# Optimization experiments

Hardware: AMD Instinct MI355X
Metric: run time of the kernel (lower is better)

The kernel has to match this reference:

```python
import jax, jax.numpy as jnp
import numpy as np

B, L, D, H, FF = 2, 2048, 1024, 16, 4096


def _xavier(key, out_d, in_d):
    lim = (6.0 / (in_d + out_d)) ** 0.5
    return jax.random.uniform(key, (out_d, in_d), jnp.float32, -lim, lim)


def setup_inputs() -> dict:
    key = jax.random.key(0)
    ks = jax.random.split(key, 7)
    x = jax.random.normal(ks[0], (B, L, D), dtype=jnp.float32)
    wq = _xavier(ks[1], D, D)
    wk = _xavier(ks[2], D, D)
    wv = _xavier(ks[3], D, D)
    wo = _xavier(ks[4], D, D)
    w1 = _xavier(ks[5], FF, D)
    w2 = _xavier(ks[6], D, FF)
    zD = jnp.zeros((D,), jnp.float32)
    return dict(x=x, wq=wq, bq=zD, wk=wk, bk=zD, wv=wv, bv=zD, wo=wo, bo=zD,
                w1=w1, b1=jnp.zeros((FF,), jnp.float32), w2=w2, b2=zD)


def _ln2d(x, eps=1e-5):
    # F.layer_norm(x, x.shape[1:]): normalize jointly over (L, D), no affine
    mu = jnp.mean(x, axis=(1, 2), keepdims=True)
    var = jnp.var(x, axis=(1, 2), keepdims=True)
    return (x - mu) * jax.lax.rsqrt(var + eps)


def reference(x, wq, bq, wk, bk, wv, bv, wo, bo, w1, b1, w2, b2):
    Bx, Lx, Dx = x.shape
    nH = H
    Dh = Dx // nH
    h = _ln2d(x)
    q = (h @ wq.T + bq).reshape(Bx, Lx, nH, Dh).transpose(0, 2, 1, 3)  # (B,H,L,Dh)
    k = (h @ wk.T + bk).reshape(Bx, Lx, nH, Dh).transpose(0, 2, 1, 3)
    v = (h @ wv.T + bv).reshape(Bx, Lx, nH, Dh).transpose(0, 2, 1, 3)
    # NOTE: faithful to source bug: scale = 1/sqrt(key.size(dim=1)) = 1/sqrt(num_heads)
    scale = 1.0 / jnp.sqrt(jnp.asarray(nH, jnp.float32))
    att = jax.nn.softmax(jnp.einsum('bhqd,bhkd->bhqk', q, k) * scale, axis=-1)
    o = jnp.einsum('bhqk,bhkd->bhqd', att, v).transpose(0, 2, 1, 3).reshape(Bx, Lx, Dx)
    o = o @ wo.T + bo
    y = _ln2d(o + x)
    ff = jax.nn.relu(y @ w1.T + b1) @ w2.T + b2
    return ff + x  # second residual adds the ORIGINAL x (as in source)
```

## Files before the change

kernel.cpp:

```cpp
#include <hip/hip_runtime.h>
#include <cstdint>
#include <cstddef>

typedef unsigned short u16;
typedef unsigned int uint;
typedef __bf16 bf16x8 __attribute__((ext_vector_type(8)));
typedef float f32x4 __attribute__((ext_vector_type(4)));

#define BATCH 2
#define SEQ 2048
#define DIM 1024
#define NH 16
#define DH 64
#define FFD 4096
#define MROWS 4096
#define PER_BATCH 2097152

__device__ __forceinline__ u16 f2b(float f) {
  uint u = __builtin_bit_cast(uint, f);
  u += 0x7FFFu + ((u >> 16) & 1u);
  return (u16)(u >> 16);
}

__device__ __forceinline__ uint pkbf2(float a, float b) {
  u16 x = __builtin_bit_cast(u16, (__bf16)a);
  u16 y = __builtin_bit_cast(u16, (__bf16)b);
  return (uint)x | ((uint)y << 16);
}

__device__ __forceinline__ int xcd_swz(int flat, int nwg) {
  return (flat & 7) * (nwg >> 3) + (flat >> 3);
}

#define GLL(gp, lp)                                                            \
  __builtin_amdgcn_global_load_lds(                                            \
      (const __attribute__((address_space(1))) void*)(gp),                     \
      (__attribute__((address_space(3))) void*)(lp), 16, 0, 0)

__global__ __launch_bounds__(256) void cvt4_kernel(const float* __restrict__ s0,
                                                   const float* __restrict__ s1,
                                                   const float* __restrict__ s2,
                                                   const float* __restrict__ s3,
                                                   u16* d0, u16* d1, u16* d2, u16* d3,
                                                   int n) {
  int t = blockIdx.y;
  const float* src = (t == 0) ? s0 : (t == 1) ? s1 : (t == 2) ? s2 : s3;
  u16* dst = (t == 0) ? d0 : (t == 1) ? d1 : (t == 2) ? d2 : d3;
  int i = (blockIdx.x * 256 + threadIdx.x) * 8;
  if (i >= n) return;
  float4 a = *(const float4*)(src + i);
  float4 b = *(const float4*)(src + i + 4);
  uint4 o;
  o.x = f2b(a.x) | ((uint)f2b(a.y) << 16);
  o.y = f2b(a.z) | ((uint)f2b(a.w) << 16);
  o.z = f2b(b.x) | ((uint)f2b(b.y) << 16);
  o.w = f2b(b.z) | ((uint)f2b(b.w) << 16);
  *(uint4*)(dst + i) = o;
}

__global__ __launch_bounds__(256) void reduce_stats_kernel(const float* __restrict__ x,
                                                           float* __restrict__ stats) {
  int b = blockIdx.y;
  const float* p = x + (size_t)b * PER_BATCH;
  float s = 0.f, ss = 0.f;
  int stride = gridDim.x * 256 * 4;
  for (int i = (blockIdx.x * 256 + threadIdx.x) * 4; i < PER_BATCH; i += stride) {
    float4 v = *(const float4*)(p + i);
    s  += (v.x + v.y) + (v.z + v.w);
    ss += (v.x * v.x + v.y * v.y) + (v.z * v.z + v.w * v.w);
  }
#pragma unroll
  for (int m = 32; m; m >>= 1) { s += __shfl_xor(s, m); ss += __shfl_xor(ss, m); }
  __shared__ float red[16];
  int w = threadIdx.x >> 6;
  if ((threadIdx.x & 63) == 0) { red[w] = s; red[8 + w] = ss; }
  __syncthreads();
  if (threadIdx.x == 0) {
    atomicAdd(&stats[b * 2],     red[0] + red[1] + red[2] + red[3]);
    atomicAdd(&stats[b * 2 + 1], red[8] + red[9] + red[10] + red[11]);
  }
}

__global__ __launch_bounds__(256) void ln_apply_kernel(const float* __restrict__ xin,
                                                       const float* __restrict__ stats,
                                                       u16* __restrict__ out) {
  int i = (blockIdx.x * 256 + threadIdx.x) * 4;
  int b = i >> 21;
  const float inv = 1.f / (float)PER_BATCH;
  float mu = stats[b * 2] * inv;
  float var = stats[b * 2 + 1] * inv - mu * mu;
  float rs = rsqrtf(var + 1e-5f);
  float4 v = *(const float4*)(xin + i);
  uint r0 = f2b((v.x - mu) * rs) | ((uint)f2b((v.y - mu) * rs) << 16);
  uint r1 = f2b((v.z - mu) * rs) | ((uint)f2b((v.w - mu) * rs) << 16);
  *(uint2*)(out + i) = make_uint2(r0, r1);
}

template <int TN, int RELU, int RESID, int OUTBF, int TRV, int DBUF>
__device__ __forceinline__ void gemm_bt_body(const u16* __restrict__ A,
                                             const u16* __restrict__ Bm,
                                             const float* __restrict__ bias,
                                             const float* __restrict__ resid,
                                             void* __restrict__ Cout,
                                             int M, int N, int K,
                                             int m0, int n0, float oscale) {
  constexpr int AI  = (TN == 128) ? 4 : 2;
  constexpr int BCH = (TN == 128) ? 4 : 2;
  constexpr int NB  = DBUF ? 2 : 1;
  __shared__ __align__(16) u16 As[NB][128 * 64];
  __shared__ __align__(16) u16 Bs[NB][TN * 64];
  const int tid = threadIdx.x;
  const int lane = tid & 63, w = tid >> 6;
  const int wr = (TN == 128) ? (w >> 1) : w;
  const int wc = (TN == 128) ? (w & 1) : 0;
  const int ln = lane & 15, qd = lane >> 4;

  f32x4 acc[AI][4] = {};

  const int lrow = lane >> 3;
  const int scl  = (lane & 7) ^ lrow;
  const u16* Ag = A  + (size_t)(m0 + w * 32 + lrow) * K + scl * 8;
  const u16* Bg = Bm + (size_t)(n0 + w * 8 * BCH + lrow) * K + scl * 8;

  const int co0 = ((qd)     ^ (ln & 7)) * 8;
  const int co1 = ((4 + qd) ^ (ln & 7)) * 8;

  auto STAGE = [&](int buf, int k0) {
#pragma unroll
    for (int r = 0; r < 4; ++r)
      GLL(Ag + (size_t)(r * 8) * K + k0, As[buf] + (w * 4 + r) * 512);
#pragma unroll
    for (int r = 0; r < BCH; ++r)
      GLL(Bg + (size_t)(r * 8) * K + k0, Bs[buf] + (w * BCH + r) * 512);
  };

  auto COMPUTE = [&](int buf) {
#pragma unroll
    for (int kk = 0; kk < 2; ++kk) {
      const int co = kk ? co1 : co0;
      bf16x8 af[AI], bf[4];
#pragma unroll
      for (int t = 0; t < AI; ++t)
        af[t] = *(const bf16x8*)&As[buf][(wr * (AI * 16) + t * 16 + ln) * 64 + co];
#pragma unroll
      for (int t = 0; t < 4; ++t)
        bf[t] = *(const bf16x8*)&Bs[buf][(wc * 64 + t * 16 + ln) * 64 + co];
#pragma unroll
      for (int i = 0; i < AI; ++i)
#pragma unroll
        for (int j = 0; j < 4; ++j)
          acc[i][j] = __builtin_amdgcn_mfma_f32_16x16x32_bf16(af[i], bf[j], acc[i][j], 0, 0, 0);
    }
  };

  if constexpr (NB == 2) {
    const int nk = K >> 6;
    STAGE(0, 0);
    for (int t = 0; t < nk; ++t) {
      const int p = t & 1;
      __syncthreads();
      if (t + 1 < nk) STAGE(1 - p, (t + 1) * 64);
      COMPUTE(p);
    }
  } else {
    for (int k0 = 0; k0 < K; k0 += 64) {
      __syncthreads();
      STAGE(0, k0);
      __syncthreads();
      COMPUTE(0);
    }
  }

#pragma unroll
  for (int i = 0; i < AI; ++i) {
    int row = m0 + wr * (AI * 16) + i * 16 + qd * 4;
#pragma unroll
    for (int j = 0; j < 4; ++j) {
      int col = n0 + wc * 64 + j * 16 + ln;
      float bv = bias[col];
      if (TRV) {
        union { uint2 u2; u16 us[4]; } pk;
#pragma unroll
        for (int r = 0; r < 4; ++r) pk.us[r] = f2b(acc[i][j][r] + bv);
        *(uint2*)&((u16*)Cout)[(size_t)col * MROWS + row] = pk.u2;
      } else {
#pragma unroll
        for (int r = 0; r < 4; ++r) {
          float v = (acc[i][j][r] + bv) * oscale;
          if (RELU) v = fmaxf(v, 0.f);
          size_t off = (size_t)(row + r) * N + col;
          if (RESID) v += resid[off];
          if (OUTBF) ((u16*)Cout)[off] = f2b(v);
          else       ((float*)Cout)[off] = v;
        }
      }
    }
  }
}

template <int TN, int RELU, int RESID, int OUTBF, int DBUF>
__global__ __launch_bounds__(256) void gemm_bt_kernel(const u16* __restrict__ A,
                                                      const u16* __restrict__ Bm,
                                                      const float* __restrict__ bias,
                                                      const float* __restrict__ resid,
                                                      void* __restrict__ Cout,
                                                      int M, int N, int K) {
  const int nx = gridDim.x;
  const int nwg = nx * gridDim.y;
  const int wid = xcd_swz(blockIdx.x + nx * blockIdx.y, nwg);
  gemm_bt_body<TN, RELU, RESID, OUTBF, 0, DBUF>(A, Bm, bias, resid, Cout, M, N, K,
                                                (wid / nx) * 128, (wid % nx) * TN, 1.0f);
}

__global__ __launch_bounds__(256) void gemm_qkv_kernel(const u16* __restrict__ A,
                                                       const u16* B0, const u16* B1, const u16* B2,
                                                       const float* c0, const float* c1, const float* c2,
                                                       u16* o0, u16* o1, u16* o2) {
  int z = blockIdx.z;
  const int wid = xcd_swz(blockIdx.x + 8 * blockIdx.y, 256);
  const int m0 = (wid >> 3) * 128, n0 = (wid & 7) * 128;
  if (z == 2) {
    gemm_bt_body<128, 0, 0, 1, 1, 0>(A, B2, c2, nullptr, o2, MROWS, DIM, DIM,
                                     m0, n0, 1.0f);
  } else {
    const u16* Bm = (z == 0) ? B0 : B1;
    const float* bias = (z == 0) ? c0 : c1;
    u16* Cout = (z == 0) ? o0 : o1;
    float sc = (z == 0) ? 0.25f : 1.0f;
    gemm_bt_body<128, 0, 0, 1, 0, 0>(A, Bm, bias, nullptr, Cout, MROWS, DIM, DIM,
                                     m0, n0, sc);
  }
}

__global__ __launch_bounds__(256, 2) void attn_kernel(const u16* __restrict__ Q,
                                                      const u16* __restrict__ Km,
                                                      const u16* __restrict__ vT,
                                                      u16* __restrict__ O) {
  __shared__ __align__(16) u16 Ks[2][64 * 64];
  __shared__ __align__(16) u16 Vt[2][64 * 64];
  __shared__ __align__(16) u16 Ps[4][32 * 64];

  const int tid = threadIdx.x, lane = tid & 63, w = tid >> 6;
  const int ln = lane & 15, qd = lane >> 4;
  const int flat = blockIdx.x + 16 * (blockIdx.y + 16 * blockIdx.z);
  const int wid = xcd_swz(flat, 512);
  const int qi = wid & 15, head = (wid >> 4) & 15, b = wid >> 8;
  const int wq0 = b * SEQ + qi * 128 + w * 32;
  const int hcol = head * DH;

  bf16x8 qf[2][2];
#pragma unroll
  for (int ti = 0; ti < 2; ++ti)
#pragma unroll
    for (int kk = 0; kk < 2; ++kk)
      qf[ti][kk] = *(const bf16x8*)&Q[(size_t)(wq0 + ti * 16 + ln) * DIM + hcol + kk * 32 + qd * 8];

  union { u16 u[8]; bf16x8 v; } oneu;
#pragma unroll
  for (int e = 0; e < 8; ++e) oneu.u[e] = 0x3F80;
  const bf16x8 vones = oneu.v;

  f32x4 accO[2][4] = {};
  f32x4 accL[2] = {};

  const int srow = lane >> 3;
  const int scl  = (lane & 7) ^ srow;
  const u16* Kg = Km + (size_t)(b * SEQ + w * 16 + srow) * DIM + hcol + scl * 8;
  const u16* Vg = vT + (size_t)(hcol + w * 16 + srow) * MROWS + b * SEQ + scl * 8;
  u16* Pw = Ps[w];
  const int swz = ln & 7;

#pragma unroll
  for (int r = 0; r < 2; ++r) {
    GLL(Kg + (size_t)(r * 8) * DIM,   &Ks[0][(w * 2 + r) * 512]);
    GLL(Vg + (size_t)(r * 8) * MROWS, &Vt[0][(w * 2 + r) * 512]);
  }

  for (int t = 0; t < SEQ / 64; ++t) {
    const int p = t & 1;
    const int kt = t * 64;
    __syncthreads();

    if (t + 1 < SEQ / 64) {
      const int kt2 = kt + 64;
#pragma unroll
      for (int r = 0; r < 2; ++r) {
        GLL(Kg + (size_t)(kt2 + r * 8) * DIM,   &Ks[1 - p][(w * 2 + r) * 512]);
        GLL(Vg + (size_t)(r * 8) * MROWS + kt2, &Vt[1 - p][(w * 2 + r) * 512]);
      }
    }

    f32x4 sacc[4][2] = {};
#pragma unroll
    for (int kk = 0; kk < 2; ++kk) {
      bf16x8 kf[4];
#pragma unroll
      for (int tj = 0; tj < 4; ++tj)
        kf[tj] = *(const bf16x8*)&Ks[p][(tj * 16 + ln) * 64 + (((kk * 4 + qd) ^ swz) * 8)];
      __builtin_amdgcn_s_setprio(1);
#pragma unroll
      for (int tj = 0; tj < 4; ++tj)
#pragma unroll
        for (int ti = 0; ti < 2; ++ti)
          sacc[tj][ti] = __builtin_amdgcn_mfma_f32_16x16x32_bf16(kf[tj], qf[ti][kk], sacc[tj][ti], 0, 0, 0);
      __builtin_amdgcn_s_setprio(0);
    }

#pragma unroll
    for (int tj = 0; tj < 4; ++tj)
#pragma unroll
      for (int ti = 0; ti < 2; ++ti) {
        uint lo = pkbf2(__expf(sacc[tj][ti][0]), __expf(sacc[tj][ti][1]));
        uint hi = pkbf2(__expf(sacc[tj][ti][2]), __expf(sacc[tj][ti][3]));
        *(uint2*)&Pw[(ti * 16 + ln) * 64 + (((2 * tj + (qd >> 1)) ^ swz) * 8) + (qd & 1) * 4] =
            make_uint2(lo, hi);
      }

#pragma unroll
    for (int kk = 0; kk < 2; ++kk) {
      bf16x8 pf[2], vf[4];
#pragma unroll
      for (int ti = 0; ti < 2; ++ti)
        pf[ti] = *(const bf16x8*)&Pw[(ti * 16 + ln) * 64 + (((kk * 4 + qd) ^ swz) * 8)];
#pragma unroll
      for (int tjv = 0; tjv < 4; ++tjv)
        vf[tjv] = *(const bf16x8*)&Vt[p][(tjv * 16 + ln) * 64 + (((kk * 4 + qd) ^ swz) * 8)];
      __builtin_amdgcn_s_setprio(1);
#pragma unroll
      for (int ti = 0; ti < 2; ++ti) {
#pragma unroll
        for (int tjv = 0; tjv < 4; ++tjv)
          accO[ti][tjv] = __builtin_amdgcn_mfma_f32_16x16x32_bf16(pf[ti], vf[tjv], accO[ti][tjv], 0, 0, 0);
        accL[ti] = __builtin_amdgcn_mfma_f32_16x16x32_bf16(pf[ti], vones, accL[ti], 0, 0, 0);
      }
      __builtin_amdgcn_s_setprio(0);
    }
  }

#pragma unroll
  for (int ti = 0; ti < 2; ++ti)
#pragma unroll
    for (int r = 0; r < 4; ++r) {
      float inv = 1.f / accL[ti][r];
#pragma unroll
      for (int tjv = 0; tjv < 4; ++tjv)
        O[(size_t)(wq0 + ti * 16 + qd * 4 + r) * DIM + hcol + tjv * 16 + ln] =
            f2b(accO[ti][tjv][r] * inv);
    }
}

extern "C" void kernel_launch(void* const* d_in, const int* in_sizes, int n_in,
                              void* d_out, int out_size, void* d_ws, size_t ws_size,
                              hipStream_t stream) {
  const float* x  = (const float*)d_in[0];
  const float* wq = (const float*)d_in[1];
  const float* bq = (const float*)d_in[2];
  const float* wk = (const float*)d_in[3];
  const float* bk = (const float*)d_in[4];
  const float* wv = (const float*)d_in[5];
  const float* bv = (const float*)d_in[6];
  const float* wo = (const float*)d_in[7];
  const float* bo = (const float*)d_in[8];
  const float* w1 = (const float*)d_in[9];
  const float* b1 = (const float*)d_in[10];
  const float* w2 = (const float*)d_in[11];
  const float* b2 = (const float*)d_in[12];
  float* out = (float*)d_out;
  char* ws = (char*)d_ws;

  const size_t MB = 1u << 20;
  u16*   h    = (u16*)(ws + 0);
  u16*   q    = (u16*)(ws + 8  * MB);
  u16*   k    = (u16*)(ws + 16 * MB);
  u16*   v    = (u16*)(ws + 24 * MB);
  u16*   o    = (u16*)(ws + 32 * MB);
  u16*   r    = (u16*)(ws + 8  * MB);
  float* ares = (float*)(ws + 40 * MB);
  u16*   wqb  = (u16*)(ws + 56 * MB);
  u16*   wkb  = (u16*)(ws + 58 * MB);
  u16*   wvb  = (u16*)(ws + 60 * MB);
  u16*   wob  = (u16*)(ws + 62 * MB);
  u16*   w1b  = (u16*)(ws + 64 * MB);
  u16*   w2b  = (u16*)(ws + 72 * MB);
  float* stats= (float*)(ws + 80 * MB);
  u16*   y    = h;

  (void)hipMemsetAsync(stats, 0, 64, stream);

  cvt4_kernel<<<dim3(512, 4),  256, 0, stream>>>(wq, wk, wv, wo, wqb, wkb, wvb, wob, DIM * DIM);
  cvt4_kernel<<<dim3(2048, 2), 256, 0, stream>>>(w1, w2, w1, w2, w1b, w2b, w1b, w2b, FFD * DIM);

  reduce_stats_kernel<<<dim3(64, 2), 256, 0, stream>>>(x, stats);
  ln_apply_kernel<<<4096, 256, 0, stream>>>(x, stats, h);

  gemm_qkv_kernel<<<dim3(8, 32, 3), 256, 0, stream>>>(h, wqb, wkb, wvb, bq, bk, bv, q, k, v);

  attn_kernel<<<dim3(16, 16, 2), 256, 0, stream>>>(q, k, v, o);

  gemm_bt_kernel<128, 0, 1, 0, 1><<<dim3(8, 32), 256, 0, stream>>>(o, wob, bo, x, ares, MROWS, DIM, DIM);

  reduce_stats_kernel<<<dim3(64, 2), 256, 0, stream>>>(ares, stats + 4);
  ln_apply_kernel<<<4096, 256, 0, stream>>>(ares, stats + 4, y);

  gemm_bt_kernel<128, 1, 0, 1, 1><<<dim3(32, 32), 256, 0, stream>>>(y, w1b, b1, nullptr, r, MROWS, FFD, DIM);
  gemm_bt_kernel<128, 0, 1, 0, 1><<<dim3(8, 32), 256, 0, stream>>>(r, w2b, b2, x, out, MROWS, DIM, FFD);
}
```

Before: 380.3 us.

## Split-K the FFN down-projection with atomics and retune Wo/W1 GEMM tiles

```diff
diff --git a/kernel.cpp b/kernel.cpp
--- a/kernel.cpp
+++ b/kernel.cpp
@@ -96,13 +96,23 @@
   *(uint2*)(out + i) = make_uint2(r0, r1);
 }
 
-template <int TN, int RELU, int RESID, int OUTBF, int TRV, int DBUF>
+__global__ __launch_bounds__(256) void init_bias_resid_kernel(const float* __restrict__ x,
+                                                              const float* __restrict__ bias,
+                                                              float* __restrict__ out) {
+  int i = (blockIdx.x * 256 + threadIdx.x) * 4;
+  float4 v = *(const float4*)(x + i);
+  float4 b = *(const float4*)(bias + (i & (DIM - 1)));
+  v.x += b.x; v.y += b.y; v.z += b.z; v.w += b.w;
+  *(float4*)(out + i) = v;
+}
+
+template <int TN, int RELU, int RESID, int OUTBF, int TRV, int DBUF, int ATOMIC>
 __device__ __forceinline__ void gemm_bt_body(const u16* __restrict__ A,
                                              const u16* __restrict__ Bm,
                                              const float* __restrict__ bias,
                                              const float* __restrict__ resid,
                                              void* __restrict__ Cout,
-                                             int M, int N, int K,
+                                             int M, int N, int K, int Kloop,
                                              int m0, int n0, float oscale) {
   constexpr int AI  = (TN == 128) ? 4 : 2;
   constexpr int BCH = (TN == 128) ? 4 : 2;
@@ -154,7 +164,7 @@
   };
 
   if constexpr (NB == 2) {
-    const int nk = K >> 6;
+    const int nk = Kloop >> 6;
     STAGE(0, 0);
     for (int t = 0; t < nk; ++t) {
       const int p = t & 1;
@@ -163,7 +173,7 @@
       COMPUTE(p);
     }
   } else {
-    for (int k0 = 0; k0 < K; k0 += 64) {
+    for (int k0 = 0; k0 < Kloop; k0 += 64) {
       __syncthreads();
       STAGE(0, k0);
       __syncthreads();
@@ -177,13 +187,18 @@
 #pragma unroll
     for (int j = 0; j < 4; ++j) {
       int col = n0 + wc * 64 + j * 16 + ln;
-      float bv = bias[col];
-      if (TRV) {
+      if (ATOMIC) {
+#pragma unroll
+        for (int r = 0; r < 4; ++r)
+          atomicAdd(&((float*)Cout)[(size_t)(row + r) * N + col], acc[i][j][r]);
+      } else if (TRV) {
+        float bv = bias[col];
         union { uint2 u2; u16 us[4]; } pk;
 #pragma unroll
         for (int r = 0; r < 4; ++r) pk.us[r] = f2b(acc[i][j][r] + bv);
         *(uint2*)&((u16*)Cout)[(size_t)col * MROWS + row] = pk.u2;
       } else {
+        float bv = bias[col];
 #pragma unroll
         for (int r = 0; r < 4; ++r) {
           float v = (acc[i][j][r] + bv) * oscale;
@@ -198,7 +213,7 @@
   }
 }
 
-template <int TN, int RELU, int RESID, int OUTBF, int DBUF>
+template <int TN, int RELU, int RESID, int OUTBF, int DBUF, int ATOMIC, int SPLITK>
 __global__ __launch_bounds__(256) void gemm_bt_kernel(const u16* __restrict__ A,
                                                       const u16* __restrict__ Bm,
                                                       const float* __restrict__ bias,
@@ -208,8 +223,11 @@
   const int nx = gridDim.x;
   const int nwg = nx * gridDim.y;
   const int wid = xcd_swz(blockIdx.x + nx * blockIdx.y, nwg);
-  gemm_bt_body<TN, RELU, RESID, OUTBF, 0, DBUF>(A, Bm, bias, resid, Cout, M, N, K,
-                                                (wid / nx) * 128, (wid % nx) * TN, 1.0f);
+  const int Ks = K / SPLITK;
+  const int ko = blockIdx.z * Ks;
+  gemm_bt_body<TN, RELU, RESID, OUTBF, 0, DBUF, ATOMIC>(
+      A + ko, Bm + ko, bias, resid, Cout, M, N, K, Ks,
+      (wid / nx) * 128, (wid % nx) * TN, 1.0f);
 }
 
 __global__ __launch_bounds__(256) void gemm_qkv_kernel(const u16* __restrict__ A,
@@ -220,15 +238,15 @@
   const int wid = xcd_swz(blockIdx.x + 8 * blockIdx.y, 256);
   const int m0 = (wid >> 3) * 128, n0 = (wid & 7) * 128;
   if (z == 2) {
-    gemm_bt_body<128, 0, 0, 1, 1, 0>(A, B2, c2, nullptr, o2, MROWS, DIM, DIM,
-                                     m0, n0, 1.0f);
+    gemm_bt_body<128, 0, 0, 1, 1, 0, 0>(A, B2, c2, nullptr, o2, MROWS, DIM, DIM, DIM,
+                                        m0, n0, 1.0f);
   } else {
     const u16* Bm = (z == 0) ? B0 : B1;
     const float* bias = (z == 0) ? c0 : c1;
     u16* Cout = (z == 0) ? o0 : o1;
     float sc = (z == 0) ? 0.25f : 1.0f;
-    gemm_bt_body<128, 0, 0, 1, 0, 0>(A, Bm, bias, nullptr, Cout, MROWS, DIM, DIM,
-                                     m0, n0, sc);
+    gemm_bt_body<128, 0, 0, 1, 0, 0, 0>(A, Bm, bias, nullptr, Cout, MROWS, DIM, DIM, DIM,
+                                        m0, n0, sc);
   }
 }
 
@@ -397,11 +415,13 @@
 
   attn_kernel<<<dim3(16, 16, 2), 256, 0, stream>>>(q, k, v, o);
 
-  gemm_bt_kernel<128, 0, 1, 0, 1><<<dim3(8, 32), 256, 0, stream>>>(o, wob, bo, x, ares, MROWS, DIM, DIM);
+  gemm_bt_kernel<64, 0, 1, 0, 1, 0, 1><<<dim3(16, 32), 256, 0, stream>>>(o, wob, bo, x, ares, MROWS, DIM, DIM);
 
   reduce_stats_kernel<<<dim3(64, 2), 256, 0, stream>>>(ares, stats + 4);
   ln_apply_kernel<<<4096, 256, 0, stream>>>(ares, stats + 4, y);
 
-  gemm_bt_kernel<128, 1, 0, 1, 1><<<dim3(32, 32), 256, 0, stream>>>(y, w1b, b1, nullptr, r, MROWS, FFD, DIM);
-  gemm_bt_kernel<128, 0, 1, 0, 1><<<dim3(8, 32), 256, 0, stream>>>(r, w2b, b2, x, out, MROWS, DIM, FFD);
-}
+  gemm_bt_kernel<128, 1, 0, 1, 0, 0, 1><<<dim3(32, 32), 256, 0, stream>>>(y, w1b, b1, nullptr, r, MROWS, FFD, DIM);
+
+  init_bias_resid_kernel<<<4096, 256, 0, stream>>>(x, b2, out);
+  gemm_bt_kernel<128, 0, 0, 0, 1, 1, 2><<<dim3(8, 32, 2), 256, 0, stream>>>(r, w2b, b2, nullptr, out, MROWS, DIM, FFD);
+}
```

Result: no change. 378.5 us (-0.5%).

## Add 256x256-tile GEMM for FFN up-projection and halve N-tile for narrow GEMMs

Applied to the files above, without the earlier changes.

```diff
diff --git a/kernel.cpp b/kernel.cpp
--- a/kernel.cpp
+++ b/kernel.cpp
@@ -212,6 +212,89 @@
                                                 (wid / nx) * 128, (wid % nx) * TN, 1.0f);
 }
 
+template <int RELU>
+__global__ __launch_bounds__(512, 2) void gemm256_kernel(const u16* __restrict__ A,
+                                                         const u16* __restrict__ Bm,
+                                                         const float* __restrict__ bias,
+                                                         u16* __restrict__ Cout,
+                                                         int M, int N, int K) {
+  __shared__ __align__(16) u16 As[2][256 * 64];
+  __shared__ __align__(16) u16 Bs[2][256 * 64];
+  const int tid = threadIdx.x;
+  const int lane = tid & 63, w = tid >> 6;
+  const int wr = w >> 2, wc = w & 3;
+  const int ln = lane & 15, qd = lane >> 4;
+
+  const int nx = gridDim.x;
+  const int nwg = nx * gridDim.y;
+  const int wid = xcd_swz(blockIdx.x + nx * blockIdx.y, nwg);
+  const int m0 = (wid / nx) * 256, n0 = (wid % nx) * 256;
+
+  f32x4 acc[8][4] = {};
+
+  const int lrow = lane >> 3;
+  const int scl  = (lane & 7) ^ lrow;
+  const u16* Ag = A  + (size_t)(m0 + w * 32 + lrow) * K + scl * 8;
+  const u16* Bg = Bm + (size_t)(n0 + w * 32 + lrow) * K + scl * 8;
+
+  const int co0 = ((qd)     ^ (ln & 7)) * 8;
+  const int co1 = ((4 + qd) ^ (ln & 7)) * 8;
+
+  auto STAGE = [&](int buf, int k0) {
+#pragma unroll
+    for (int r = 0; r < 4; ++r) {
+      GLL(Ag + (size_t)(r * 8) * K + k0, As[buf] + (w * 4 + r) * 512);
+      GLL(Bg + (size_t)(r * 8) * K + k0, Bs[buf] + (w * 4 + r) * 512);
+    }
+  };
+
+  auto COMPUTE = [&](int buf) {
+#pragma unroll
+    for (int kk = 0; kk < 2; ++kk) {
+      const int co = kk ? co1 : co0;
+      bf16x8 af[8], bf[4];
+#pragma unroll
+      for (int t = 0; t < 8; ++t)
+        af[t] = *(const bf16x8*)&As[buf][(wr * 128 + t * 16 + ln) * 64 + co];
+#pragma unroll
+      for (int t = 0; t < 4; ++t)
+        bf[t] = *(const bf16x8*)&Bs[buf][(wc * 64 + t * 16 + ln) * 64 + co];
+      __builtin_amdgcn_s_setprio(1);
+#pragma unroll
+      for (int i = 0; i < 8; ++i)
+#pragma unroll
+        for (int j = 0; j < 4; ++j)
+          acc[i][j] = __builtin_amdgcn_mfma_f32_16x16x32_bf16(af[i], bf[j], acc[i][j], 0, 0, 0);
+      __builtin_amdgcn_s_setprio(0);
+    }
+  };
+
+  const int nk = K >> 6;
+  STAGE(0, 0);
+  for (int t = 0; t < nk; ++t) {
+    const int p = t & 1;
+    __syncthreads();
+    if (t + 1 < nk) STAGE(1 - p, (t + 1) * 64);
+    COMPUTE(p);
+  }
+
+#pragma unroll
+  for (int i = 0; i < 8; ++i) {
+    int row = m0 + wr * 128 + i * 16 + qd * 4;
+#pragma unroll
+    for (int j = 0; j < 4; ++j) {
+      int col = n0 + wc * 64 + j * 16 + ln;
+      float bv = bias[col];
+#pragma unroll
+      for (int r = 0; r < 4; ++r) {
+        float v = acc[i][j][r] + bv;
+        if (RELU) v = fmaxf(v, 0.f);
+        Cout[(size_t)(row + r) * N + col] = f2b(v);
+      }
+    }
+  }
+}
+
 __global__ __launch_bounds__(256) void gemm_qkv_kernel(const u16* __restrict__ A,
                                                        const u16* B0, const u16* B1, const u16* B2,
                                                        const float* c0, const float* c1, const float* c2,
@@ -397,11 +480,12 @@
 
   attn_kernel<<<dim3(16, 16, 2), 256, 0, stream>>>(q, k, v, o);
 
-  gemm_bt_kernel<128, 0, 1, 0, 1><<<dim3(8, 32), 256, 0, stream>>>(o, wob, bo, x, ares, MROWS, DIM, DIM);
+  gemm_bt_kernel<64, 0, 1, 0, 1><<<dim3(16, 32), 256, 0, stream>>>(o, wob, bo, x, ares, MROWS, DIM, DIM);
 
   reduce_stats_kernel<<<dim3(64, 2), 256, 0, stream>>>(ares, stats + 4);
   ln_apply_kernel<<<4096, 256, 0, stream>>>(ares, stats + 4, y);
 
-  gemm_bt_kernel<128, 1, 0, 1, 1><<<dim3(32, 32), 256, 0, stream>>>(y, w1b, b1, nullptr, r, MROWS, FFD, DIM);
-  gemm_bt_kernel<128, 0, 1, 0, 1><<<dim3(8, 32), 256, 0, stream>>>(r, w2b, b2, x, out, MROWS, DIM, FFD);
-}
+  gemm256_kernel<1><<<dim3(16, 16), 512, 0, stream>>>(y, w1b, b1, r, MROWS, FFD, DIM);
+
+  gemm_bt_kernel<64, 0, 1, 0, 1><<<dim3(16, 32), 256, 0, stream>>>(r, w2b, b2, x, out, MROWS, DIM, FFD);
+}
```

Result: faster. 357.6 us (-6.0%).
